# Kernel tuning notes

Hardware: AMD Instinct MI355X
Metric: run time of the kernel (lower is better)

Reference implementation:

```python
import jax, jax.numpy as jnp
import numpy as np

D_G = 16384; B = 128; NNZ = 262144
CL1_F = 32; CL1_K = 6; FC1_F = 512; FC2_F = 512
NN_FC1 = 512; NN_FC2 = 256
CL4_F = 32; CL4_K = 4; FC1_G4 = 128; FC2_G4 = 64
OUT = 10; POOL1 = 8; POOL4 = 3; V4 = 10; EMB = 64
FC1FIN = CL1_F * (D_G // POOL1)        # 65536
G4OUT = CL4_F * (OUT // POOL4)         # 96
SUMFIN = FC1_F + NN_FC2 + FC2_G4 + 64  # 896


def _cheby(x, W, b, spmm, K):
    # x: [B, V, Fin]; Chebyshev recursion T_k(L) x with K-order feature stacking
    Bb, V, Fin = x.shape
    x0 = jnp.transpose(x, (1, 2, 0)).reshape(V, Fin * Bb)
    xs = [x0]
    if K > 1:
        x1 = spmm(x0)
        xs.append(x1)
        for _ in range(K - 2):
            x2 = 2.0 * spmm(x1) - x0
            xs.append(x2)
            x0, x1 = x1, x2
    X = jnp.stack(xs).reshape(K, V, Fin, Bb)
    X = jnp.transpose(X, (3, 1, 2, 0)).reshape(Bb * V, Fin * K)  # [B*V, Fin*K]
    return (X @ W.T + b).reshape(Bb, V, -1)


def _gmaxpool(x, p):
    # MaxPool1d(p) over node dim (floor truncation like torch)
    Bb, V, F = x.shape
    Vp = (V // p) * p
    return x[:, :Vp].reshape(Bb, V // p, p, F).max(axis=2)


def setup_inputs():
    key = jax.random.key(0)
    ks = jax.random.split(key, 32)
    def lin(i, fo, fi):
        return (jax.random.normal(ks[i], (fo, fi), jnp.float32) * 0.02,
                jnp.zeros((fo,), jnp.float32))
    cl1_W, cl1_b = lin(0, CL1_F, CL1_K)
    fc1_W, fc1_b = lin(1, FC1_F, FC1FIN)
    fc2_W, fc2_b = lin(2, FC2_F, FC1_F)
    fc3_W, fc3_b = lin(3, D_G, FC2_F)
    nn1_W, nn1_b = lin(4, NN_FC1, D_G)
    nn2_W, nn2_b = lin(5, NN_FC2, NN_FC1)
    cl4_W, cl4_b = lin(6, CL4_F, CL4_K * EMB)
    fcg1_W, fcg1_b = lin(7, FC1_G4, G4OUT)
    fcg2_W, fcg2_b = lin(8, FC2_G4, FC1_G4)
    nn14_W, nn14_b = lin(9, 256, V4 * EMB)
    nn24_W, nn24_b = lin(10, 64, 256)
    fcsum_W, fcsum_b = lin(11, OUT, SUMFIN)
    return {
        'x_in': jax.random.normal(ks[12], (B, D_G), jnp.float32),
        'x_embed': jax.random.normal(ks[13], (V4, EMB), jnp.float32),
        'dropout': 0,
        'L_rows': jnp.sort(jax.random.randint(ks[14], (NNZ,), 0, D_G)),
        'L_cols': jax.random.randint(ks[15], (NNZ,), 0, D_G),
        'L_vals': jax.random.normal(ks[16], (NNZ,), jnp.float32) * 0.1,
        'L_mg': jax.random.normal(ks[17], (V4, V4), jnp.float32) * 0.2,
        'cl1_W': cl1_W, 'cl1_b': cl1_b, 'fc1_W': fc1_W, 'fc1_b': fc1_b,
        'fc2_W': fc2_W, 'fc2_b': fc2_b, 'fc3_W': fc3_W, 'fc3_b': fc3_b,
        'nn1_W': nn1_W, 'nn1_b': nn1_b, 'nn2_W': nn2_W, 'nn2_b': nn2_b,
        'cl4_W': cl4_W, 'cl4_b': cl4_b, 'fcg1_W': fcg1_W, 'fcg1_b': fcg1_b,
        'fcg2_W': fcg2_W, 'fcg2_b': fcg2_b, 'nn14_W': nn14_W, 'nn14_b': nn14_b,
        'nn24_W': nn24_W, 'nn24_b': nn24_b, 'fcsum_W': fcsum_W, 'fcsum_b': fcsum_b,
    }


def reference(x_in, x_embed, dropout, L_rows, L_cols, L_vals, L_mg,
              cl1_W, cl1_b, fc1_W, fc1_b, fc2_W, fc2_b, fc3_W, fc3_b,
              nn1_W, nn1_b, nn2_W, nn2_b, cl4_W, cl4_b,
              fcg1_W, fcg1_b, fcg2_W, fcg2_b, nn14_W, nn14_b, nn24_W, nn24_b,
              fcsum_W, fcsum_b):
    Bb = x_in.shape[0]
    def spmm_L(m):  # COO SpMM: y[r] += v * m[c]
        return jax.ops.segment_sum(L_vals[:, None] * m[L_cols], L_rows,
                                   num_segments=D_G)
    # --- GCN 1 (gene graph) ---
    x = _cheby(x_in[:, :, None], cl1_W, cl1_b, spmm_L, CL1_K)
    x = jax.nn.relu(x)
    x = _gmaxpool(x, POOL1).reshape(Bb, FC1FIN)
    x_hidden_gae = jax.nn.relu(x @ fc1_W.T + fc1_b)
    # FC2_F != 0 branch; dropout p=0 is identity at this baseline
    x_decode_gae = jax.nn.relu(x_hidden_gae @ fc2_W.T + fc2_b)
    x_decode_gae = x_decode_gae @ fc3_W.T + fc3_b
    # --- NN 1 ---
    x_nn = jax.nn.relu(x_in @ nn1_W.T + nn1_b)
    x_nn = jax.nn.relu(x_nn @ nn2_W.T + nn2_b)
    # --- GCN 4 (small meta-graph, dense Laplacian) ---
    xe = jnp.broadcast_to(x_embed[None], (Bb, V4, EMB))
    xg = _cheby(xe, cl4_W, cl4_b, lambda m: L_mg @ m, CL4_K)
    xg = jax.nn.relu(xg)
    xg = _gmaxpool(xg, POOL4).reshape(Bb, G4OUT)
    xg = jax.nn.relu(xg @ fcg1_W.T + fcg1_b)
    xg = jax.nn.relu(xg @ fcg2_W.T + fcg2_b)
    # --- NN of GCN4 ---
    xn4 = xe.reshape(Bb, V4 * EMB)
    xn4 = jax.nn.relu(xn4 @ nn14_W.T + nn14_b)
    xn4 = jax.nn.relu(xn4 @ nn24_W.T + nn24_b)
    data_emb = jnp.concatenate([x_hidden_gae, x_nn, xg, xn4], axis=1)
    logp = jax.nn.log_softmax(data_emb @ fcsum_W.T + fcsum_b, axis=-1)
    return x_decode_gae, x_hidden_gae, logp
```

## Files before the change

kernel.cpp:

```cpp
#include <hip/hip_runtime.h>
#include <hip/hip_bf16.h>

#define DG 16384
#define NNZ 262144
#define BB 128

typedef __attribute__((ext_vector_type(8))) short bf16x8;
typedef __attribute__((ext_vector_type(8))) unsigned short us8;
typedef __attribute__((ext_vector_type(4))) float f32x4;
typedef __attribute__((ext_vector_type(4))) unsigned short us4;
typedef __attribute__((ext_vector_type(2))) float f32x2;

#define WS_ROWPTR 0
#define WS_XIN16  66048
#define WS_T      4260352
#define WS_XPOOL  54592000
#define WS_XB0    71369216
#define WS_XB1    75563520
#define WS_XNN1B  79757824
#define WS_DEC2   79888896
#define WS_XNN2   80019968
#define WS_HIDB   80151040
#define WS_N1     80282112
#define WS_TAIL   80283136
#define PART_NN1_OFF 0
#define PART_FC1_OFF 8388608

__device__ __forceinline__ unsigned short f2bf(float f) {
  __hip_bfloat16 h = __float2bfloat16(f);
  return __builtin_bit_cast(unsigned short, h);
}
__device__ __forceinline__ float bflo(unsigned u) {
  return __builtin_bit_cast(float, u << 16);
}
__device__ __forceinline__ float bfhi(unsigned u) {
  return __builtin_bit_cast(float, u & 0xffff0000u);
}

__device__ void prep_dev(const float* __restrict__ x_in, const int* __restrict__ rows,
                         int* __restrict__ rowptr, unsigned short* __restrict__ xin16,
                         int bid) {
  int idx = bid * 256 + threadIdx.x;
  if (idx <= DG) {
    int lo = 0, hi = NNZ;
    while (lo < hi) { int mid = (lo + hi) >> 1; if (rows[mid] < idx) lo = mid + 1; else hi = mid; }
    rowptr[idx] = lo;
  }
  f32x4 v = ((const f32x4*)x_in)[idx];
  us4 o; o[0] = f2bf(v[0]); o[1] = f2bf(v[1]); o[2] = f2bf(v[2]); o[3] = f2bf(v[3]);
  ((us4*)xin16)[idx] = o;
}

__device__ void transpose_dev(const float* __restrict__ x_in, float* __restrict__ T0,
                              unsigned short* __restrict__ Xb0, int id) {
  __shared__ float tl[32][33];
  int bx = id & 511, by = id >> 9;
  int v0 = bx * 32, b0 = by * 32;
  int tx = threadIdx.x & 31, ty0 = threadIdx.x >> 5;
  #pragma unroll
  for (int j = 0; j < 4; ++j) {
    int ty = ty0 + j * 8;
    tl[ty][tx] = x_in[(size_t)(b0 + ty) * DG + v0 + tx];
  }
  __syncthreads();
  #pragma unroll
  for (int j = 0; j < 4; ++j) {
    int ty = ty0 + j * 8;
    float v = tl[tx][ty];
    size_t o = (size_t)(v0 + ty) * BB + b0 + tx;
    T0[o] = v;
    Xb0[o] = f2bf(v);
  }
}

__device__ void dot4_dev(const float* __restrict__ x, const float* __restrict__ W,
                         const float* __restrict__ bias, float* __restrict__ out,
                         int K, int id) {
  int w = threadIdx.x >> 6, lane = threadIdx.x & 63;
  int o = id * 4 + w;
  float a = 0.f;
  for (int i = lane; i < K; i += 64) a += x[i] * W[(size_t)o * K + i];
  #pragma unroll
  for (int s = 32; s > 0; s >>= 1) a += __shfl_down(a, s);
  if (lane == 0) out[o] = fmaxf(a + bias[o], 0.f);
}

__device__ void g4_dev(const float* __restrict__ xe_g, const float* __restrict__ Lmg_g,
                       const float* __restrict__ W4, const float* __restrict__ b4,
                       const float* __restrict__ Wg1, const float* __restrict__ bg1,
                       const float* __restrict__ Wg2, const float* __restrict__ bg2,
                       float* __restrict__ tail) {
  __shared__ float Lm[100], Tg[4][640], xc[320], xg96[96], h1[128];
  int t = threadIdx.x;
  for (int i = t; i < 640; i += 256) Tg[0][i] = xe_g[i];
  for (int i = t; i < 100; i += 256) Lm[i] = Lmg_g[i];
  __syncthreads();
  for (int i = t; i < 640; i += 256) {
    int v = i >> 6, f = i & 63; float s = 0.f;
    #pragma unroll
    for (int u = 0; u < 10; ++u) s += Lm[v * 10 + u] * Tg[0][u * 64 + f];
    Tg[1][i] = s;
  }
  __syncthreads();
  for (int kk = 2; kk < 4; ++kk) {
    for (int i = t; i < 640; i += 256) {
      int v = i >> 6, f = i & 63; float s = 0.f;
      #pragma unroll
      for (int u = 0; u < 10; ++u) s += Lm[v * 10 + u] * Tg[kk - 1][u * 64 + f];
      Tg[kk][i] = 2.f * s - Tg[kk - 2][i];
    }
    __syncthreads();
  }
  for (int i = t; i < 320; i += 256) {
    int v = i >> 5, fo = i & 31; float s = b4[fo];
    for (int fin = 0; fin < 64; ++fin)
      #pragma unroll
      for (int k = 0; k < 4; ++k) s += Tg[k][v * 64 + fin] * W4[fo * 256 + fin * 4 + k];
    xc[i] = fmaxf(s, 0.f);
  }
  __syncthreads();
  for (int i = t; i < 96; i += 256) {
    int g = i >> 5, fo = i & 31;
    xg96[i] = fmaxf(fmaxf(xc[(3 * g) * 32 + fo], xc[(3 * g + 1) * 32 + fo]),
                    xc[(3 * g + 2) * 32 + fo]);
  }
  __syncthreads();
  for (int o = t; o < 128; o += 256) {
    float s = bg1[o];
    for (int i2 = 0; i2 < 96; ++i2) s += xg96[i2] * Wg1[o * 96 + i2];
    h1[o] = fmaxf(s, 0.f);
  }
  __syncthreads();
  for (int o = t; o < 64; o += 256) {
    float s = bg2[o];
    for (int i2 = 0; i2 < 128; ++i2) s += h1[i2] * Wg2[o * 128 + i2];
    tail[o] = fmaxf(s, 0.f);
  }
}

__global__ __launch_bounds__(256) void setup_kernel(
    const float* __restrict__ x_in, const int* __restrict__ rows,
    int* __restrict__ rowptr, unsigned short* __restrict__ xin16,
    float* __restrict__ T0, unsigned short* __restrict__ Xb0,
    const float* __restrict__ x_embed,
    const float* __restrict__ nn14_W, const float* __restrict__ nn14_b,
    float* __restrict__ n1,
    const float* __restrict__ Lmg, const float* __restrict__ W4,
    const float* __restrict__ b4, const float* __restrict__ Wg1,
    const float* __restrict__ bg1, const float* __restrict__ Wg2,
    const float* __restrict__ bg2, float* __restrict__ tail) {
  int bid = blockIdx.x;
  if (bid < 1) g4_dev(x_embed, Lmg, W4, b4, Wg1, bg1, Wg2, bg2, tail);
  else if (bid < 65) dot4_dev(x_embed, nn14_W, nn14_b, n1, 640, bid - 1);
  else if (bid < 2113) prep_dev(x_in, rows, rowptr, xin16, bid - 65);
  else transpose_dev(x_in, T0, Xb0, bid - 2113);
}

__global__ __launch_bounds__(256) void spmm3(
    const int* __restrict__ rowptr, const int* __restrict__ cols,
    const float* __restrict__ vals, const unsigned* __restrict__ X2,
    const float* __restrict__ Tprev, float* __restrict__ Tout,
    unsigned* __restrict__ Xbout, float scale) {
  int r = blockIdx.x * 4 + (threadIdx.x >> 6);
  int lane = threadIdx.x & 63;
  int e0 = rowptr[r], e1 = rowptr[r + 1];
  float a00 = 0.f, a01 = 0.f, a10 = 0.f, a11 = 0.f;
  int e = e0;
  for (; e + 4 <= e1; e += 4) {
    int c0 = cols[e], c1 = cols[e + 1], c2 = cols[e + 2], c3 = cols[e + 3];
    float v0 = vals[e], v1 = vals[e + 1], v2 = vals[e + 2], v3 = vals[e + 3];
    unsigned x0 = X2[c0 * 64 + lane], x1 = X2[c1 * 64 + lane];
    unsigned x2 = X2[c2 * 64 + lane], x3 = X2[c3 * 64 + lane];
    a00 += v0 * bflo(x0); a10 += v0 * bfhi(x0);
    a01 += v1 * bflo(x1); a11 += v1 * bfhi(x1);
    a00 += v2 * bflo(x2); a10 += v2 * bfhi(x2);
    a01 += v3 * bflo(x3); a11 += v3 * bfhi(x3);
  }
  for (; e < e1; ++e) {
    float v = vals[e]; unsigned x = X2[cols[e] * 64 + lane];
    a00 += v * bflo(x); a10 += v * bfhi(x);
  }
  float s0 = scale * (a00 + a01), s1 = scale * (a10 + a11);
  size_t o = (size_t)r * BB + lane * 2;
  if (Tprev) { f32x2 p = *(const f32x2*)(Tprev + o); s0 -= p[0]; s1 -= p[1]; }
  *(f32x2*)(Tout + o) = (f32x2){s0, s1};
  Xbout[(size_t)r * 64 + lane] = (unsigned)f2bf(s0) | ((unsigned)f2bf(s1) << 16);
}

__device__ void combine_dev(const float* __restrict__ Tbase, const float* __restrict__ W,
                            const float* __restrict__ bias, unsigned short* __restrict__ xpool,
                            int vp) {
  __shared__ float tile[6][8][128];
  __shared__ float Wl[192];
  __shared__ float bl[32];
  for (int i = threadIdx.x; i < 192; i += 256) Wl[i] = W[i];
  if (threadIdx.x < 32) bl[threadIdx.x] = bias[threadIdx.x];
  for (int i = threadIdx.x; i < 6144; i += 256) {
    int k = i >> 10, rem = i & 1023, j = rem >> 7, b = rem & 127;
    tile[k][j][b] = Tbase[(size_t)k * 2097152 + (size_t)(vp * 8 + j) * BB + b];
  }
  __syncthreads();
  for (int p = threadIdx.x; p < 4096; p += 256) {
    int b = p >> 5, f = p & 31;
    float m = -1e30f;
    #pragma unroll
    for (int j = 0; j < 8; ++j) {
      float s = bl[f];
      #pragma unroll
      for (int k = 0; k < 6; ++k) s += tile[k][j][b] * Wl[f * 6 + k];
      m = fmaxf(m, s);
    }
    m = fmaxf(m, 0.f);
    xpool[(size_t)b * 65536 + vp * 32 + f] = f2bf(m);
  }
}

__global__ __launch_bounds__(256) void combine_nn24(
    const float* __restrict__ Tbase, const float* __restrict__ W,
    const float* __restrict__ bias, unsigned short* __restrict__ xpool,
    const float* __restrict__ n1, const float* __restrict__ nn24_W,
    const float* __restrict__ nn24_b, float* __restrict__ tail64) {
  int bid = blockIdx.x;
  if (bid < 2048) combine_dev(Tbase, W, bias, xpool, bid);
  else dot4_dev(n1, nn24_W, nn24_b, tail64, 256, bid - 2048);
}

template<int NT, int MT>
__device__ void gemm_core3(
    unsigned short* __restrict__ Alds,
    unsigned short* __restrict__ Wlds,
    const unsigned short* __restrict__ A, const float* __restrict__ W,
    float* __restrict__ outP, unsigned short* __restrict__ outB,
    const float* __restrict__ bias, int K, int N, int Kchunk,
    int bx, int by, int row0, int relu, int partial) {
  const int LA = MT / 2;
  const int LW = NT * 4;
  int t = threadIdx.x, w = t >> 6, lane = t & 63, lr = lane & 15, lg = lane >> 4;
  int n0 = bx * NT * 64;
  int kbeg = by * Kchunk;
  f32x4 acc[MT][NT];
  #pragma unroll
  for (int mt = 0; mt < MT; ++mt)
    #pragma unroll
    for (int nt = 0; nt < NT; ++nt) acc[mt][nt] = (f32x4){0.f, 0.f, 0.f, 0.f};
  int rowA[LA], kkA[LA], rowW[LW], kkW[LW];
  #pragma unroll
  for (int j = 0; j < LA; ++j) { int idx = j * 256 + t; rowA[j] = idx >> 3; kkA[j] = (idx & 7) * 8; }
  #pragma unroll
  for (int j = 0; j < LW; ++j) { int idx = j * 256 + t; rowW[j] = idx >> 4; kkW[j] = (idx & 15) * 4; }
  us8 ra[LA]; f32x4 rw[LW];
  #pragma unroll
  for (int j = 0; j < LA; ++j)
    ra[j] = *(const us8*)(A + (size_t)(row0 + rowA[j]) * K + kbeg + kkA[j]);
  #pragma unroll
  for (int j = 0; j < LW; ++j)
    rw[j] = *(const f32x4*)(W + (size_t)(n0 + rowW[j]) * K + kbeg + kkW[j]);
  int stages = Kchunk >> 6;
  for (int s = 0; s < stages; ++s) {
    __syncthreads();
    #pragma unroll
    for (int j = 0; j < LA; ++j)
      *(us8*)(Alds + rowA[j] * 64 + (kkA[j] ^ ((rowA[j] & 7) << 3))) = ra[j];
    #pragma unroll
    for (int j = 0; j < LW; ++j) {
      us4 o; o[0] = f2bf(rw[j][0]); o[1] = f2bf(rw[j][1]);
      o[2] = f2bf(rw[j][2]); o[3] = f2bf(rw[j][3]);
      *(us4*)(Wlds + rowW[j] * 64 + (kkW[j] ^ ((rowW[j] & 7) << 3))) = o;
    }
    if (s + 1 < stages) {
      int k0 = kbeg + (s + 1) * 64;
      #pragma unroll
      for (int j = 0; j < LA; ++j)
        ra[j] = *(const us8*)(A + (size_t)(row0 + rowA[j]) * K + k0 + kkA[j]);
      #pragma unroll
      for (int j = 0; j < LW; ++j)
        rw[j] = *(const f32x4*)(W + (size_t)(n0 + rowW[j]) * K + k0 + kkW[j]);
    }
    __syncthreads();
    #pragma unroll
    for (int h = 0; h < 2; ++h) {
      int k32 = h * 32;
      bf16x8 bfr[NT];
      #pragma unroll
      for (int nt = 0; nt < NT; ++nt) {
        int wrow = w * NT * 16 + nt * 16 + lr;
        bfr[nt] = *(const bf16x8*)(Wlds + wrow * 64 + ((k32 + lg * 8) ^ ((wrow & 7) << 3)));
      }
      #pragma unroll
      for (int mt = 0; mt < MT; ++mt) {
        int arow = mt * 16 + lr;
        bf16x8 af = *(const bf16x8*)(Alds + arow * 64 + ((k32 + lg * 8) ^ ((arow & 7) << 3)));
        #pragma unroll
        for (int nt = 0; nt < NT; ++nt)
          acc[mt][nt] = __builtin_amdgcn_mfma_f32_16x16x32_bf16(af, bfr[nt], acc[mt][nt], 0, 0, 0);
      }
    }
  }
  if (partial) {
    float* P = outP + (size_t)by * 128 * (size_t)N;
    #pragma unroll
    for (int mt = 0; mt < MT; ++mt)
      #pragma unroll
      for (int nt = 0; nt < NT; ++nt) {
        int col = n0 + w * NT * 16 + nt * 16 + lr;
        #pragma unroll
        for (int r2 = 0; r2 < 4; ++r2) {
          int row = row0 + mt * 16 + lg * 4 + r2;
          P[(size_t)row * N + col] = acc[mt][nt][r2];
        }
      }
  } else {
    #pragma unroll
    for (int mt = 0; mt < MT; ++mt)
      #pragma unroll
      for (int nt = 0; nt < NT; ++nt) {
        int col = n0 + w * NT * 16 + nt * 16 + lr;
        float bc = bias[col];
        #pragma unroll
        for (int r2 = 0; r2 < 4; ++r2) {
          int row = row0 + mt * 16 + lg * 4 + r2;
          float v = acc[mt][nt][r2] + bc;
          if (relu) v = fmaxf(v, 0.f);
          if (outP) outP[(size_t)row * N + col] = v;
          if (outB) outB[(size_t)row * N + col] = f2bf(v);
        }
      }
  }
}

__global__ __launch_bounds__(256) void gemm_partials(
    const unsigned short* __restrict__ xin16, const float* __restrict__ nn1_W,
    const unsigned short* __restrict__ xpool, const float* __restrict__ fc1_W,
    float* __restrict__ pnn1, float* __restrict__ pfc1) {
  __shared__ unsigned short Alds[128 * 64];
  __shared__ unsigned short Wlds[128 * 64];
  int nb = blockIdx.x;
  if (nb < 128) {
    int xcd = nb & 7, q = nb >> 3, bx = q & 3, by = ((q >> 2) << 3) | xcd;
    gemm_core3<2, 8>(Alds, Wlds, xin16, nn1_W, pnn1, nullptr, nullptr,
                     16384, 512, 512, bx, by, 0, 0, 1);
  } else {
    int b = nb - 128;
    int xcd = b & 7, q = b >> 3, bx = q & 3, by = ((q >> 2) << 3) | xcd;
    gemm_core3<2, 8>(Alds, Wlds, xpool, fc1_W, pfc1, nullptr, nullptr,
                     65536, 512, 512, bx, by, 0, 0, 1);
  }
}

__global__ __launch_bounds__(256) void reduce_fused(
    const float* __restrict__ pfc1, const float* __restrict__ fc1_b,
    float* __restrict__ hidden, unsigned short* __restrict__ hidB,
    const float* __restrict__ pnn1, const float* __restrict__ nn1_b,
    unsigned short* __restrict__ xnn1b) {
  int b = blockIdx.x;
  if (b < 256) {
    int idx = b * 256 + threadIdx.x;
    float s = 0.f;
    for (int i = 0; i < 128; ++i) s += pfc1[(size_t)i * 65536 + idx];
    float v = fmaxf(s + fc1_b[idx & 511], 0.f);
    hidden[idx] = v;
    hidB[idx] = f2bf(v);
  } else {
    int idx = (b - 256) * 256 + threadIdx.x;
    float s = 0.f;
    for (int i = 0; i < 32; ++i) s += pnn1[(size_t)i * 65536 + idx];
    float v = fmaxf(s + nn1_b[idx & 511], 0.f);
    xnn1b[idx] = f2bf(v);
  }
}

__global__ __launch_bounds__(256) void fc2nn2_kernel(
    const unsigned short* __restrict__ hidB, const float* __restrict__ fc2_W,
    const float* __restrict__ fc2_b, unsigned short* __restrict__ dec2,
    const unsigned short* __restrict__ xnn1b, const float* __restrict__ nn2_W,
    const float* __restrict__ nn2_b, float* __restrict__ xnn2) {
  __shared__ unsigned short Alds[128 * 64];
  __shared__ unsigned short Wlds[64 * 64];
  int b = blockIdx.x;
  if (b < 8)
    gemm_core3<1, 8>(Alds, Wlds, hidB, fc2_W, nullptr, dec2, fc2_b,
                     512, 512, 512, b, 0, 0, 1, 0);
  else
    gemm_core3<1, 8>(Alds, Wlds, xnn1b, nn2_W, xnn2, nullptr, nn2_b,
                     512, 256, 512, b - 8, 0, 0, 1, 0);
}

__device__ void fcsum_dev(int id, const float* __restrict__ hidden,
                          const float* __restrict__ xnn2, const float* __restrict__ tail,
                          const float* __restrict__ Ws, const float* __restrict__ bs,
                          float* __restrict__ logp) {
  __shared__ float emb[4][896];
  int w = threadIdx.x >> 6, lane = threadIdx.x & 63;
  int b = id * 4 + w;
  for (int i = lane; i < 896; i += 64)
    emb[w][i] = (i < 512) ? hidden[b * 512 + i]
              : (i < 768) ? xnn2[b * 256 + (i - 512)]
                          : tail[i - 768];
  __syncthreads();
  float l[10];
  #pragma unroll
  for (int o = 0; o < 10; ++o) {
    float a = 0.f;
    for (int i = lane; i < 896; i += 64) a += emb[w][i] * Ws[o * 896 + i];
    #pragma unroll
    for (int s = 32; s > 0; s >>= 1) a += __shfl_down(a, s);
    l[o] = __shfl(a, 0) + bs[o];
  }
  float m = l[0];
  #pragma unroll
  for (int o = 1; o < 10; ++o) m = fmaxf(m, l[o]);
  float sum = 0.f;
  #pragma unroll
  for (int o = 0; o < 10; ++o) sum += expf(l[o] - m);
  float lse = m + logf(sum);
  #pragma unroll
  for (int o = 0; o < 10; ++o)
    if (lane == o) logp[b * 10 + o] = l[o] - lse;
}

__global__ __launch_bounds__(256) void fc3_head(
    const unsigned short* __restrict__ dec2, const float* __restrict__ fc3_W,
    const float* __restrict__ fc3_b, float* __restrict__ out0,
    const float* __restrict__ hidden, const float* __restrict__ xnn2,
    const float* __restrict__ tail, const float* __restrict__ fcsum_W,
    const float* __restrict__ fcsum_b, float* __restrict__ logp) {
  __shared__ unsigned short Alds[64 * 64];
  __shared__ unsigned short Wlds[64 * 64];
  int b = blockIdx.x;
  if (b < 512) {
    int bx = b >> 1, my = b & 1;
    gemm_core3<1, 4>(Alds, Wlds, dec2, fc3_W, out0, nullptr, fc3_b,
                     512, 16384, 512, bx, 0, my * 64, 0, 0);
  } else {
    fcsum_dev(b - 512, hidden, xnn2, tail, fcsum_W, fcsum_b, logp);
  }
}

extern "C" void kernel_launch(void* const* d_in, const int* in_sizes, int n_in,
                              void* d_out, int out_size, void* d_ws, size_t ws_size,
                              hipStream_t stream) {
  const float* x_in    = (const float*)d_in[0];
  const float* x_embed = (const float*)d_in[1];
  const int*   L_rows  = (const int*)d_in[3];
  const int*   L_cols  = (const int*)d_in[4];
  const float* L_vals  = (const float*)d_in[5];
  const float* L_mg    = (const float*)d_in[6];
  const float* cl1_W = (const float*)d_in[7],  *cl1_b = (const float*)d_in[8];
  const float* fc1_W = (const float*)d_in[9],  *fc1_b = (const float*)d_in[10];
  const float* fc2_W = (const float*)d_in[11], *fc2_b = (const float*)d_in[12];
  const float* fc3_W = (const float*)d_in[13], *fc3_b = (const float*)d_in[14];
  const float* nn1_W = (const float*)d_in[15], *nn1_b = (const float*)d_in[16];
  const float* nn2_W = (const float*)d_in[17], *nn2_b = (const float*)d_in[18];
  const float* cl4_W = (const float*)d_in[19], *cl4_b = (const float*)d_in[20];
  const float* fcg1_W = (const float*)d_in[21], *fcg1_b = (const float*)d_in[22];
  const float* fcg2_W = (const float*)d_in[23], *fcg2_b = (const float*)d_in[24];
  const float* nn14_W = (const float*)d_in[25], *nn14_b = (const float*)d_in[26];
  const float* nn24_W = (const float*)d_in[27], *nn24_b = (const float*)d_in[28];
  const float* fcsum_W = (const float*)d_in[29], *fcsum_b = (const float*)d_in[30];

  char* ws = (char*)d_ws;
  int* rowptr = (int*)(ws + WS_ROWPTR);
  unsigned short* xin16 = (unsigned short*)(ws + WS_XIN16);
  float* T = (float*)(ws + WS_T);
  unsigned short* xpool = (unsigned short*)(ws + WS_XPOOL);
  unsigned short* Xb0 = (unsigned short*)(ws + WS_XB0);
  unsigned short* Xb1 = (unsigned short*)(ws + WS_XB1);
  unsigned short* xnn1b = (unsigned short*)(ws + WS_XNN1B);
  unsigned short* dec2 = (unsigned short*)(ws + WS_DEC2);
  float* xnn2 = (float*)(ws + WS_XNN2);
  unsigned short* hidB = (unsigned short*)(ws + WS_HIDB);
  float* n1 = (float*)(ws + WS_N1);
  float* tail = (float*)(ws + WS_TAIL);
  float* pnn1 = (float*)(ws + WS_T + PART_NN1_OFF);
  float* pfc1 = (float*)(ws + WS_T + PART_FC1_OFF);

  float* out0 = (float*)d_out;
  float* hidden = out0 + 2097152;
  float* logp = out0 + 2097152 + 65536;

  setup_kernel<<<4161, 256, 0, stream>>>(x_in, L_rows, rowptr, xin16, T, Xb0,
                                         x_embed, nn14_W, nn14_b, n1,
                                         L_mg, cl4_W, cl4_b, fcg1_W, fcg1_b,
                                         fcg2_W, fcg2_b, tail);

  spmm3<<<4096, 256, 0, stream>>>(rowptr, L_cols, L_vals, (const unsigned*)Xb0,
                                  nullptr,          T + 1 * 2097152, (unsigned*)Xb1, 1.f);
  spmm3<<<4096, 256, 0, stream>>>(rowptr, L_cols, L_vals, (const unsigned*)Xb1,
                                  T,                T + 2 * 2097152, (unsigned*)Xb0, 2.f);
  spmm3<<<4096, 256, 0, stream>>>(rowptr, L_cols, L_vals, (const unsigned*)Xb0,
                                  T + 1 * 2097152,  T + 3 * 2097152, (unsigned*)Xb1, 2.f);
  spmm3<<<4096, 256, 0, stream>>>(rowptr, L_cols, L_vals, (const unsigned*)Xb1,
                                  T + 2 * 2097152,  T + 4 * 2097152, (unsigned*)Xb0, 2.f);
  spmm3<<<4096, 256, 0, stream>>>(rowptr, L_cols, L_vals, (const unsigned*)Xb0,
                                  T + 3 * 2097152,  T + 5 * 2097152, (unsigned*)Xb1, 2.f);

  combine_nn24<<<2064, 256, 0, stream>>>(T, cl1_W, cl1_b, xpool,
                                         n1, nn24_W, nn24_b, tail + 64);

  gemm_partials<<<640, 256, 0, stream>>>(xin16, nn1_W, xpool, fc1_W, pnn1, pfc1);

  reduce_fused<<<512, 256, 0, stream>>>(pfc1, fc1_b, hidden, hidB,
                                        pnn1, nn1_b, xnn1b);

  fc2nn2_kernel<<<12, 256, 0, stream>>>(hidB, fc2_W, fc2_b, dec2,
                                        xnn1b, nn2_W, nn2_b, xnn2);

  fc3_head<<<544, 256, 0, stream>>>(dec2, fc3_W, fc3_b, out0,
                                    hidden, xnn2, tail, fcsum_W, fcsum_b, logp);
}
```

Before: 282.8 us.

## Drop register prefetch in GEMM core, double split-K and fc3 block counts

Removes the register-staged global prefetch from the shared GEMM core so each stage loads straight into LDS, which cuts register pressure and may raise occupancy. In exchange, load latency is no longer overlapped with the MFMA work of the previous stage. It also halves the K chunk of the nn1/fc1 split-K GEMMs, doubling the grid and the number of partial sums the reduce kernel must read. The fc3 tiles shrink from 64 to 32 rows, doubling the block count, and the partials move to dedicated workspace regions so they no longer alias T.

Measured after the change: 317.1 us. 1.12x slower.

```diff
diff --git a/kernel.cpp b/kernel.cpp
--- a/kernel.cpp
+++ b/kernel.cpp
@@ -23,8 +23,8 @@
 #define WS_HIDB   80151040
 #define WS_N1     80282112
 #define WS_TAIL   80283136
-#define PART_NN1_OFF 0
-#define PART_FC1_OFF 8388608
+#define WS_PNN1   81000448
+#define WS_PFC1   97777664
 
 __device__ __forceinline__ unsigned short f2bf(float f) {
   __hip_bfloat16 h = __float2bfloat16(f);
@@ -226,7 +226,7 @@
 }
 
 template<int NT, int MT>
-__device__ void gemm_core3(
+__device__ void gemm_core4(
     unsigned short* __restrict__ Alds,
     unsigned short* __restrict__ Wlds,
     const unsigned short* __restrict__ A, const float* __restrict__ W,
@@ -248,33 +248,20 @@
   for (int j = 0; j < LA; ++j) { int idx = j * 256 + t; rowA[j] = idx >> 3; kkA[j] = (idx & 7) * 8; }
   #pragma unroll
   for (int j = 0; j < LW; ++j) { int idx = j * 256 + t; rowW[j] = idx >> 4; kkW[j] = (idx & 15) * 4; }
-  us8 ra[LA]; f32x4 rw[LW];
-  #pragma unroll
-  for (int j = 0; j < LA; ++j)
-    ra[j] = *(const us8*)(A + (size_t)(row0 + rowA[j]) * K + kbeg + kkA[j]);
-  #pragma unroll
-  for (int j = 0; j < LW; ++j)
-    rw[j] = *(const f32x4*)(W + (size_t)(n0 + rowW[j]) * K + kbeg + kkW[j]);
   int stages = Kchunk >> 6;
   for (int s = 0; s < stages; ++s) {
+    int k0 = kbeg + s * 64;
     __syncthreads();
     #pragma unroll
-    for (int j = 0; j < LA; ++j)
-      *(us8*)(Alds + rowA[j] * 64 + (kkA[j] ^ ((rowA[j] & 7) << 3))) = ra[j];
+    for (int j = 0; j < LA; ++j) {
+      us8 v = *(const us8*)(A + (size_t)(row0 + rowA[j]) * K + k0 + kkA[j]);
+      *(us8*)(Alds + rowA[j] * 64 + (kkA[j] ^ ((rowA[j] & 7) << 3))) = v;
+    }
     #pragma unroll
     for (int j = 0; j < LW; ++j) {
-      us4 o; o[0] = f2bf(rw[j][0]); o[1] = f2bf(rw[j][1]);
-      o[2] = f2bf(rw[j][2]); o[3] = f2bf(rw[j][3]);
+      f32x4 v = *(const f32x4*)(W + (size_t)(n0 + rowW[j]) * K + k0 + kkW[j]);
+      us4 o; o[0] = f2bf(v[0]); o[1] = f2bf(v[1]); o[2] = f2bf(v[2]); o[3] = f2bf(v[3]);
       *(us4*)(Wlds + rowW[j] * 64 + (kkW[j] ^ ((rowW[j] & 7) << 3))) = o;
-    }
-    if (s + 1 < stages) {
-      int k0 = kbeg + (s + 1) * 64;
-      #pragma unroll
-      for (int j = 0; j < LA; ++j)
-        ra[j] = *(const us8*)(A + (size_t)(row0 + rowA[j]) * K + k0 + kkA[j]);
-      #pragma unroll
-      for (int j = 0; j < LW; ++j)
-        rw[j] = *(const f32x4*)(W + (size_t)(n0 + rowW[j]) * K + k0 + kkW[j]);
     }
     __syncthreads();
     #pragma unroll
@@ -335,15 +322,15 @@
   __shared__ unsigned short Alds[128 * 64];
   __shared__ unsigned short Wlds[128 * 64];
   int nb = blockIdx.x;
-  if (nb < 128) {
+  if (nb < 256) {
     int xcd = nb & 7, q = nb >> 3, bx = q & 3, by = ((q >> 2) << 3) | xcd;
-    gemm_core3<2, 8>(Alds, Wlds, xin16, nn1_W, pnn1, nullptr, nullptr,
-                     16384, 512, 512, bx, by, 0, 0, 1);
+    gemm_core4<2, 8>(Alds, Wlds, xin16, nn1_W, pnn1, nullptr, nullptr,
+                     16384, 512, 256, bx, by, 0, 0, 1);
   } else {
-    int b = nb - 128;
+    int b = nb - 256;
     int xcd = b & 7, q = b >> 3, bx = q & 3, by = ((q >> 2) << 3) | xcd;
-    gemm_core3<2, 8>(Alds, Wlds, xpool, fc1_W, pfc1, nullptr, nullptr,
-                     65536, 512, 512, bx, by, 0, 0, 1);
+    gemm_core4<2, 8>(Alds, Wlds, xpool, fc1_W, pfc1, nullptr, nullptr,
+                     65536, 512, 256, bx, by, 0, 0, 1);
   }
 }
 
@@ -356,14 +343,14 @@
   if (b < 256) {
     int idx = b * 256 + threadIdx.x;
     float s = 0.f;
-    for (int i = 0; i < 128; ++i) s += pfc1[(size_t)i * 65536 + idx];
+    for (int i = 0; i < 256; ++i) s += pfc1[(size_t)i * 65536 + idx];
     float v = fmaxf(s + fc1_b[idx & 511], 0.f);
     hidden[idx] = v;
     hidB[idx] = f2bf(v);
   } else {
     int idx = (b - 256) * 256 + threadIdx.x;
     float s = 0.f;
-    for (int i = 0; i < 32; ++i) s += pnn1[(size_t)i * 65536 + idx];
+    for (int i = 0; i < 64; ++i) s += pnn1[(size_t)i * 65536 + idx];
     float v = fmaxf(s + nn1_b[idx & 511], 0.f);
     xnn1b[idx] = f2bf(v);
   }
@@ -378,10 +365,10 @@
   __shared__ unsigned short Wlds[64 * 64];
   int b = blockIdx.x;
   if (b < 8)
-    gemm_core3<1, 8>(Alds, Wlds, hidB, fc2_W, nullptr, dec2, fc2_b,
+    gemm_core4<1, 8>(Alds, Wlds, hidB, fc2_W, nullptr, dec2, fc2_b,
                      512, 512, 512, b, 0, 0, 1, 0);
   else
-    gemm_core3<1, 8>(Alds, Wlds, xnn1b, nn2_W, xnn2, nullptr, nn2_b,
+    gemm_core4<1, 8>(Alds, Wlds, xnn1b, nn2_W, xnn2, nullptr, nn2_b,
                      512, 256, 512, b - 8, 0, 0, 1, 0);
 }
 
@@ -427,12 +414,12 @@
   __shared__ unsigned short Alds[64 * 64];
   __shared__ unsigned short Wlds[64 * 64];
   int b = blockIdx.x;
-  if (b < 512) {
-    int bx = b >> 1, my = b & 1;
-    gemm_core3<1, 4>(Alds, Wlds, dec2, fc3_W, out0, nullptr, fc3_b,
-                     512, 16384, 512, bx, 0, my * 64, 0, 0);
+  if (b < 1024) {
+    int bx = b >> 2, my = b & 3;
+    gemm_core4<1, 2>(Alds, Wlds, dec2, fc3_W, out0, nullptr, fc3_b,
+                     512, 16384, 512, bx, 0, my * 32, 0, 0);
   } else {
-    fcsum_dev(b - 512, hidden, xnn2, tail, fcsum_W, fcsum_b, logp);
+    fcsum_dev(b - 1024, hidden, xnn2, tail, fcsum_W, fcsum_b, logp);
   }
 }
 
@@ -471,8 +458,8 @@
   unsigned short* hidB = (unsigned short*)(ws + WS_HIDB);
   float* n1 = (float*)(ws + WS_N1);
   float* tail = (float*)(ws + WS_TAIL);
-  float* pnn1 = (float*)(ws + WS_T + PART_NN1_OFF);
-  float* pfc1 = (float*)(ws + WS_T + PART_FC1_OFF);
+  float* pnn1 = (float*)(ws + WS_PNN1);
+  float* pfc1 = (float*)(ws + WS_PFC1);
 
   float* out0 = (float*)d_out;
   float* hidden = out0 + 2097152;
@@ -497,7 +484,7 @@
   combine_nn24<<<2064, 256, 0, stream>>>(T, cl1_W, cl1_b, xpool,
                                          n1, nn24_W, nn24_b, tail + 64);
 
-  gemm_partials<<<640, 256, 0, stream>>>(xin16, nn1_W, xpool, fc1_W, pnn1, pfc1);
+  gemm_partials<<<1280, 256, 0, stream>>>(xin16, nn1_W, xpool, fc1_W, pnn1, pfc1);
 
   reduce_fused<<<512, 256, 0, stream>>>(pfc1, fc1_b, hidden, hidB,
                                         pnn1, nn1_b, xnn1b);
@@ -505,6 +492,6 @@
   fc2nn2_kernel<<<12, 256, 0, stream>>>(hidB, fc2_W, fc2_b, dec2,
                                         xnn1b, nn2_W, nn2_b, xnn2);
 
-  fc3_head<<<544, 256, 0, stream>>>(dec2, fc3_W, fc3_b, out0,
-                                    hidden, xnn2, tail, fcsum_W, fcsum_b, logp);
-}
+  fc3_head<<<1056, 256, 0, stream>>>(dec2, fc3_W, fc3_b, out0,
+                                     hidden, xnn2, tail, fcsum_W, fcsum_b, logp);
+}
```
